# Optimization experiments

Hardware: AMD Instinct MI355X
Metric: run time of the kernel (lower is better)

Reference implementation:

```python
import jax, jax.numpy as jnp
import numpy as np

B, T_IN, T_OUT, IN_DIM, H = 65536, 30, 30, 3, 128


def _cell(xt, h, c, Wih, Whh, b):
    # PyTorch LSTM gate order: i, f, g, o
    g = xt @ Wih.T + h @ Whh.T + b  # [B, 4H]
    i, f, gg, o = jnp.split(g, 4, axis=-1)
    i = jax.nn.sigmoid(i)
    f = jax.nn.sigmoid(f)
    gg = jnp.tanh(gg)
    o = jax.nn.sigmoid(o)
    c = f * c + i * gg
    h = o * jnp.tanh(c)
    return h, c


def setup_inputs() -> dict:
    key = jax.random.key(0)
    ks = jax.random.split(key, 20)
    s = 1.0 / np.sqrt(H)
    def u(k, shape):
        return jax.random.uniform(k, shape, jnp.float32, -s, s)
    inp = {
        "x": jax.random.normal(ks[0], (B, T_IN, IN_DIM), jnp.float32),
        "enc_Wih0": u(ks[1], (4 * H, IN_DIM)),
        "enc_Whh0": u(ks[2], (4 * H, H)),
        "enc_b0": u(ks[3], (4 * H,)),
        "enc_Wih1": u(ks[4], (4 * H, H)),
        "enc_Whh1": u(ks[5], (4 * H, H)),
        "enc_b1": u(ks[6], (4 * H,)),
        "dec_Wih0": u(ks[7], (4 * H, IN_DIM)),
        "dec_Whh0": u(ks[8], (4 * H, H)),
        "dec_b0": u(ks[9], (4 * H,)),
        "dec_Wih1": u(ks[10], (4 * H, H)),
        "dec_Whh1": u(ks[11], (4 * H, H)),
        "dec_b1": u(ks[12], (4 * H,)),
        "fc_W": u(ks[13], (2 * IN_DIM, H)),
        "fc_b": u(ks[14], (2 * IN_DIM,)),
    }
    return inp


def reference(x, enc_Wih0, enc_Whh0, enc_b0, enc_Wih1, enc_Whh1, enc_b1,
              dec_Wih0, dec_Whh0, dec_b0, dec_Wih1, dec_Whh1, dec_b1,
              fc_W, fc_b):
    Bn = x.shape[0]
    z = jnp.zeros((Bn, H), x.dtype)

    # ----- encoder: 2-layer LSTM over T_in steps, keep final (h, c) -----
    def enc_step(carry, xt):
        h0, c0, h1, c1 = carry
        h0, c0 = _cell(xt, h0, c0, enc_Wih0, enc_Whh0, enc_b0)
        h1, c1 = _cell(h0, h1, c1, enc_Wih1, enc_Whh1, enc_b1)
        return (h0, c0, h1, c1), None

    xs = jnp.swapaxes(x, 0, 1)  # [T_in, B, 3]
    (h0, c0, h1, c1), _ = jax.lax.scan(enc_step, (z, z, z, z), xs)

    def dec_step(carry, _):
        h0, c0, h1, c1, inp = carry
        h0, c0 = _cell(inp, h0, c0, dec_Wih0, dec_Whh0, dec_b0)
        h1, c1 = _cell(h0, h1, c1, dec_Wih1, dec_Whh1, dec_b1)
        stats = h1 @ fc_W.T + fc_b  # [B, 6]
        mu, logvar = jnp.split(stats, 2, axis=-1)
        return (h0, c0, h1, c1, mu), (mu, logvar)

    init = (h0, c0, h1, c1, x[:, -1, :])
    _, (mus, logvars) = jax.lax.scan(dec_step, init, None, length=T_OUT)
    mu = jnp.swapaxes(mus, 0, 1)       # [B, T_out, 3]
    logvar = jnp.swapaxes(logvars, 0, 1)
    return mu, logvar
```

## Files before the change

### kernel.cpp

```cpp
#include <hip/hip_runtime.h>
#include <cstdint>

typedef short short8  __attribute__((ext_vector_type(8)));
typedef unsigned short ushort4v __attribute__((ext_vector_type(4)));
typedef float floatx4 __attribute__((ext_vector_type(4)));

#define HID    128
#define NB     32
#define TPB    512
#define NBLK   2048
#define TSTEPS 30
#define MU_OFF 5898240
#define HSZ    4096

#define L0_SZ  81920
#define L1_SZ  131072
#define ENC0_HI 0
#define ENC0_LO 81920
#define ENC1_HI 163840
#define ENC1_LO 294912
#define DEC0_HI 425984
#define DEC0_LO 507904
#define DEC1_HI 589824
#define DEC1_LO 720896

__device__ __forceinline__ float sigm(float v){
  return __builtin_amdgcn_rcpf(1.f + __expf(-v));
}
__device__ __forceinline__ float tanh_fast(float v){
  return 2.f*__builtin_amdgcn_rcpf(1.f + __expf(-2.f*v)) - 1.f;
}

__device__ __forceinline__ unsigned short f2bf(float f){
  unsigned u = __float_as_uint(f);
  u = (u + 0x7FFF + ((u>>16)&1)) >> 16;
  return (unsigned short)u;
}
__device__ __forceinline__ float bf2f(unsigned short b){
  return __uint_as_float(((unsigned)b)<<16);
}

extern "C" __global__ void __launch_bounds__(256)
prep_frag(const float* __restrict__ eWih0, const float* __restrict__ eWhh0,
          const float* __restrict__ eWih1, const float* __restrict__ eWhh1,
          const float* __restrict__ dWih0, const float* __restrict__ dWhh0,
          const float* __restrict__ dWih1, const float* __restrict__ dWhh1,
          unsigned short* __restrict__ ws)
{
  const int idx = blockIdx.x*256 + threadIdx.x;
  int i2, hi_base, lo_base, KT;
  const float* Wa; const float* Wb;
  if (idx < L0_SZ)                { i2=idx;                 hi_base=ENC0_HI; lo_base=ENC0_LO; Wa=eWhh0; Wb=eWih0; KT=5; }
  else if (idx < L0_SZ+L1_SZ)     { i2=idx-L0_SZ;           hi_base=ENC1_HI; lo_base=ENC1_LO; Wa=eWih1; Wb=eWhh1; KT=8; }
  else if (idx < 2*L0_SZ+L1_SZ)   { i2=idx-(L0_SZ+L1_SZ);   hi_base=DEC0_HI; lo_base=DEC0_LO; Wa=dWhh0; Wb=dWih0; KT=5; }
  else                            { i2=idx-(2*L0_SZ+L1_SZ); hi_base=DEC1_HI; lo_base=DEC1_LO; Wa=dWih1; Wb=dWhh1; KT=8; }
  const int jj = i2 & 7, l = (i2>>3)&63, tk = i2>>9;
  const int kt = (KT==5) ? (tk%5) : (tk&7);
  const int mt = (KT==5) ? (tk/5) : (tk>>3);
  const int row = mt*16 + (l&15);
  const int k   = kt*32 + ((l>>4)&3)*8 + jj;
  float w;
  if (KT==5) w = (k<128) ? Wa[row*128+k] : ((k<131) ? Wb[row*3 + (k-128)] : 0.f);
  else       w = (k<128) ? Wa[row*128+k] : Wb[row*128 + (k-128)];
  const unsigned short hi = f2bf(w);
  ws[hi_base + i2] = hi;
  ws[lo_base + i2] = f2bf(w - bf2f(hi));
}

extern "C" __global__ void __launch_bounds__(TPB, 4)
lstm_mfma(const float* __restrict__ x,
          const unsigned short* __restrict__ wf,
          const float* __restrict__ enc_b0, const float* __restrict__ enc_b1,
          const float* __restrict__ dec_b0, const float* __restrict__ dec_b1,
          const float* __restrict__ fc_W,  const float* __restrict__ fc_b,
          float* __restrict__ out)
{
  __shared__ unsigned short h0h[2*HSZ];
  __shared__ unsigned short h1h[2*HSZ];
  __shared__ unsigned short xbh[2*NB*8], xbl[2*NB*8];
  __shared__ unsigned short fcAh[4*512], fcAl[4*512];
  __shared__ float bias[1024];

  const int tid  = threadIdx.x;
  const int w    = tid>>6, l = tid&63;
  const int quad = (l>>4)&3, n15 = l&15;
  const int b0   = blockIdx.x*NB;

  bias[tid]       = enc_b0[tid];
  bias[512 + tid] = enc_b1[tid];
  for (int i=tid;i<2*HSZ;i+=TPB){ h0h[i]=0; h1h[i]=0; }
  xbh[tid]=0; xbl[tid]=0;
  if (w < 4){
    short8 vh, vl;
#pragma unroll
    for (int jj=0;jj<8;jj++){
      const float f = (n15<6) ? fc_W[n15*HID + w*32 + quad*8 + jj] : 0.f;
      const unsigned short hi = f2bf(f);
      vh[jj] = (short)hi;
      vl[jj] = (short)f2bf(f - bf2f(hi));
    }
    *(short8*)(fcAh + (w*64+l)*8) = vh;
    *(short8*)(fcAl + (w*64+l)*8) = vl;
  }
  float myfcb[4];
#pragma unroll
  for (int r=0;r<4;r++){
    const int oi = quad*4 + r;
    myfcb[r] = (oi<6) ? fc_b[oi] : 0.f;
  }
  __syncthreads();

  auto write_x = [&](int t, int p){
    if (tid < 96){
      const int n = tid & 31, c = tid >> 5;
      const float v = x[(size_t)(b0+n)*90 + t*3 + c];
      const unsigned short hi = f2bf(v);
      xbh[p*256 + n*8 + c] = hi;
      xbl[p*256 + n*8 + c] = f2bf(v - bf2f(hi));
    }
  };
  write_x(0, 0);
  __syncthreads();

  floatx4 acc[4][2];
  float c0[2][4], c1[2][4];
#pragma unroll
  for (int nt=0;nt<2;nt++)
#pragma unroll
    for (int r=0;r<4;r++){ c0[nt][r]=0.f; c1[nt][r]=0.f; }

  auto zacc = [&]{
    const floatx4 z = {0.f,0.f,0.f,0.f};
#pragma unroll
    for (int g=0;g<4;g++){ acc[g][0]=z; acc[g][1]=z; }
  };

  auto mv = [&](const unsigned short* __restrict__ Ahi, int KT,
                int k0, int k1, int kboff,
                const unsigned short* Bh){
#pragma unroll 1
    for (int kt=k0; kt<k1; ++kt){
      const int bo = ((((kt-kboff)*4+quad)^n15)<<3);
      short8 bh[2];
#pragma unroll
      for (int nt=0;nt<2;nt++){
        const int ro = (nt*16+n15)*128 + bo;
        bh[nt] = *(const short8*)(Bh + ro);
      }
      short8 ah[4];
#pragma unroll
      for (int g=0;g<4;g++){
        const int ao = (((g*8+w)*KT + kt)*64 + l)*8;
        ah[g] = *(const short8*)(Ahi + ao);
      }
#pragma unroll
      for (int g=0;g<4;g++){
        acc[g][0] = __builtin_amdgcn_mfma_f32_16x16x32_bf16(ah[g], bh[0], acc[g][0],0,0,0);
        acc[g][1] = __builtin_amdgcn_mfma_f32_16x16x32_bf16(ah[g], bh[1], acc[g][1],0,0,0);
      }
    }
  };

  auto mv_x = [&](const unsigned short* __restrict__ Ahi,
                  const unsigned short* Xh, const unsigned short* Xl){
    const short8 z8 = {0,0,0,0,0,0,0,0};
    short8 bh[2]={z8,z8}, bl[2]={z8,z8};
    if (quad==0){
#pragma unroll
      for (int nt=0;nt<2;nt++){
        const int ro = (nt*16+n15)*8;
        bh[nt] = *(const short8*)(Xh + ro);
        bl[nt] = *(const short8*)(Xl + ro);
      }
    }
    short8 ah[4];
#pragma unroll
    for (int g=0;g<4;g++){
      const int ao = (((g*8+w)*5 + 4)*64 + l)*8;
      ah[g] = *(const short8*)(Ahi + ao);
    }
#pragma unroll
    for (int g=0;g<4;g++){
      acc[g][0] = __builtin_amdgcn_mfma_f32_16x16x32_bf16(ah[g], bh[0], acc[g][0],0,0,0);
      acc[g][1] = __builtin_amdgcn_mfma_f32_16x16x32_bf16(ah[g], bh[1], acc[g][1],0,0,0);
    }
#pragma unroll
    for (int g=0;g<4;g++){
      acc[g][0] = __builtin_amdgcn_mfma_f32_16x16x32_bf16(ah[g], bl[0], acc[g][0],0,0,0);
      acc[g][1] = __builtin_amdgcn_mfma_f32_16x16x32_bf16(ah[g], bl[1], acc[g][1],0,0,0);
    }
  };

  auto cell = [&](float (&cst)[2][4], int boff, unsigned short* Hh){
    float hv[2][4];
#pragma unroll
    for (int nt=0;nt<2;nt++)
#pragma unroll
      for (int r=0;r<4;r++){
        const int j = w*16 + quad*4 + r;
        const float i_ = sigm(acc[0][nt][r]      + bias[boff       + j]);
        const float f_ = sigm(acc[1][nt][r]      + bias[boff + 128 + j]);
        const float g_ = tanh_fast(acc[2][nt][r] + bias[boff + 256 + j]);
        const float o_ = sigm(acc[3][nt][r]      + bias[boff + 384 + j]);
        const float c  = f_*cst[nt][r] + i_*g_;
        cst[nt][r] = c;
        hv[nt][r]  = o_*tanh_fast(c);
      }
#pragma unroll
    for (int nt=0;nt<2;nt++){
      const int jb = w*2 + (quad>>1);
      const int n  = nt*16 + n15;
      const int base = n*128 + ((jb ^ n15)<<3) + ((quad&1)<<2);
      ushort4v ph;
#pragma unroll
      for (int r=0;r<4;r++) ph[r] = f2bf(hv[nt][r]);
      *(ushort4v*)(Hh + base) = ph;
    }
  };

  auto fc = [&](int t, const unsigned short* Hh1, int xp){
    if (w < 2){
      floatx4 fa = {0.f,0.f,0.f,0.f};
#pragma unroll
      for (int kt=0;kt<4;kt++){
        const short8 ah = *(const short8*)(fcAh + (kt*64+l)*8);
        const short8 al = *(const short8*)(fcAl + (kt*64+l)*8);
        const int bo = (((kt*4+quad)^n15)<<3);
        const int ro = (w*16+n15)*128 + bo;
        const short8 bh = *(const short8*)(Hh1 + ro);
        fa = __builtin_amdgcn_mfma_f32_16x16x32_bf16(ah, bh, fa,0,0,0);
        fa = __builtin_amdgcn_mfma_f32_16x16x32_bf16(al, bh, fa,0,0,0);
      }
      const int n = w*16 + n15;
      const size_t off = (size_t)(b0+n)*90 + (size_t)t*3;
      if (quad == 0){
#pragma unroll
        for (int r=0;r<4;r++){
          const float s = fa[r] + myfcb[r];
          if (r < 3){
            out[off + r] = s;
            const unsigned short hi = f2bf(s);
            xbh[xp*256 + n*8 + r] = hi;
            xbl[xp*256 + n*8 + r] = f2bf(s - bf2f(hi));
          } else {
            out[MU_OFF + off] = s;
          }
        }
      } else if (quad == 1){
#pragma unroll
        for (int r=0;r<2;r++)
          out[MU_OFF + off + 1 + r] = fa[r] + myfcb[r];
      }
    }
  };

#pragma unroll 1
  for (int t=0; t<TSTEPS; ++t){
    const int ra = (t&1)*HSZ,  wa = HSZ - ra;
    const int xr = (t&1)*256;
    zacc();
    mv  (wf+ENC0_HI, 5, 0, 4, 0, h0h+ra);
    mv_x(wf+ENC0_HI, xbh+xr, xbl+xr);
    cell(c0, 0, h0h+wa);
    if (t+1 < TSTEPS) write_x(t+1, (t+1)&1);
    __syncthreads();
    zacc();
    mv(wf+ENC1_HI, 8, 0, 4, 0, h0h+wa);
    mv(wf+ENC1_HI, 8, 4, 8, 4, h1h+ra);
    cell(c1, 512, h1h+wa);
    __syncthreads();
  }

  bias[tid]       = dec_b0[tid];
  bias[512 + tid] = dec_b1[tid];
  __syncthreads();

#pragma unroll 1
  for (int t=0; t<TSTEPS; ++t){
    const int ra = (t&1)*HSZ,  wa = HSZ - ra;
    const int xw = (t&1)*256,  xr = 256 - xw;
    zacc();
    mv  (wf+DEC0_HI, 5, 0, 4, 0, h0h+ra);
    mv_x(wf+DEC0_HI, xbh+xr, xbl+xr);
    cell(c0, 0, h0h+wa);
    __syncthreads();
    zacc();
    mv(wf+DEC1_HI, 8, 0, 4, 0, h0h+wa);
    mv(wf+DEC1_HI, 8, 4, 8, 4, h1h+ra);
    cell(c1, 512, h1h+wa);
    __syncthreads();
    fc(t, h1h+wa, t&1);
    __syncthreads();
  }
}

extern "C" void kernel_launch(void* const* d_in, const int* in_sizes, int n_in,
                              void* d_out, int out_size, void* d_ws, size_t ws_size,
                              hipStream_t stream) {
  const float* x        = (const float*)d_in[0];
  const float* enc_Wih0 = (const float*)d_in[1];
  const float* enc_Whh0 = (const float*)d_in[2];
  const float* enc_b0   = (const float*)d_in[3];
  const float* enc_Wih1 = (const float*)d_in[4];
  const float* enc_Whh1 = (const float*)d_in[5];
  const float* enc_b1   = (const float*)d_in[6];
  const float* dec_Wih0 = (const float*)d_in[7];
  const float* dec_Whh0 = (const float*)d_in[8];
  const float* dec_b0   = (const float*)d_in[9];
  const float* dec_Wih1 = (const float*)d_in[10];
  const float* dec_Whh1 = (const float*)d_in[11];
  const float* dec_b1   = (const float*)d_in[12];
  const float* fc_W     = (const float*)d_in[13];
  const float* fc_b     = (const float*)d_in[14];
  unsigned short* ws = (unsigned short*)d_ws;
  float* out = (float*)d_out;

  prep_frag<<<1664, 256, 0, stream>>>(
      enc_Wih0, enc_Whh0, enc_Wih1, enc_Whh1,
      dec_Wih0, dec_Whh0, dec_Wih1, dec_Whh1, ws);

  lstm_mfma<<<NBLK, TPB, 0, stream>>>(
      x, ws, enc_b0, enc_b1, dec_b0, dec_b1, fc_W, fc_b, out);
}
```

Baseline: 2.657 ms.

## Reorder weight fragments per wave, cache biases in registers, pack bf16 conversion

Weight fragments are re-laid out so that each wave's four gate A-fragments for a k-tile sit contiguously, which simplifies address arithmetic in the inner loops. Gate biases are held in per-thread registers instead of being read from LDS in every cell. The h-state conversion now uses the hardware v_cvt_pk_bf16_f32 instruction, and s_setprio is raised around the MFMA bursts. These changes increase register pressure under the 4-block launch bound, and the hardware conversion's rounding may differ slightly from the manual round-to-nearest-even.

```diff
diff --git a/kernel.cpp b/kernel.cpp
--- a/kernel.cpp
+++ b/kernel.cpp
@@ -3,6 +3,7 @@
 
 typedef short short8  __attribute__((ext_vector_type(8)));
 typedef unsigned short ushort4v __attribute__((ext_vector_type(4)));
+typedef unsigned int uint2v __attribute__((ext_vector_type(2)));
 typedef float floatx4 __attribute__((ext_vector_type(4)));
 
 #define HID    128
@@ -38,6 +39,11 @@
 }
 __device__ __forceinline__ float bf2f(unsigned short b){
   return __uint_as_float(((unsigned)b)<<16);
+}
+__device__ __forceinline__ unsigned cvt_pk_bf16(float lo, float hi){
+  unsigned r;
+  asm("v_cvt_pk_bf16_f32 %0, %1, %2" : "=v"(r) : "v"(lo), "v"(hi));
+  return r;
 }
 
 extern "C" __global__ void __launch_bounds__(256)
@@ -63,8 +69,10 @@
   if (KT==5) w = (k<128) ? Wa[row*128+k] : ((k<131) ? Wb[row*3 + (k-128)] : 0.f);
   else       w = (k<128) ? Wa[row*128+k] : Wb[row*128 + (k-128)];
   const unsigned short hi = f2bf(w);
-  ws[hi_base + i2] = hi;
-  ws[lo_base + i2] = f2bf(w - bf2f(hi));
+  const int w8 = mt & 7, g = mt >> 3;
+  const int oidx = (((w8*KT + kt)*4 + g)*512) + l*8 + jj;
+  ws[hi_base + oidx] = hi;
+  ws[lo_base + oidx] = f2bf(w - bf2f(hi));
 }
 
 extern "C" __global__ void __launch_bounds__(TPB, 4)
@@ -110,6 +118,19 @@
   }
   __syncthreads();
 
+  float myb0[4][4], myb1[4][4];
+  auto load_myb = [&]{
+#pragma unroll
+    for (int g=0;g<4;g++)
+#pragma unroll
+      for (int r=0;r<4;r++){
+        const int j = g*128 + w*16 + quad*4 + r;
+        myb0[g][r] = bias[j];
+        myb1[g][r] = bias[512 + j];
+      }
+  };
+  load_myb();
+
   auto write_x = [&](int t, int p){
     if (tid < 96){
       const int n = tid & 31, c = tid >> 5;
@@ -147,17 +168,18 @@
         const int ro = (nt*16+n15)*128 + bo;
         bh[nt] = *(const short8*)(Bh + ro);
       }
+      const unsigned short* Aw = Ahi + ((w*KT + kt)*4)*512 + l*8;
       short8 ah[4];
 #pragma unroll
-      for (int g=0;g<4;g++){
-        const int ao = (((g*8+w)*KT + kt)*64 + l)*8;
-        ah[g] = *(const short8*)(Ahi + ao);
-      }
+      for (int g=0;g<4;g++)
+        ah[g] = *(const short8*)(Aw + g*512);
+      __builtin_amdgcn_s_setprio(1);
 #pragma unroll
       for (int g=0;g<4;g++){
         acc[g][0] = __builtin_amdgcn_mfma_f32_16x16x32_bf16(ah[g], bh[0], acc[g][0],0,0,0);
         acc[g][1] = __builtin_amdgcn_mfma_f32_16x16x32_bf16(ah[g], bh[1], acc[g][1],0,0,0);
       }
+      __builtin_amdgcn_s_setprio(0);
     }
   };
 
@@ -173,12 +195,12 @@
         bl[nt] = *(const short8*)(Xl + ro);
       }
     }
+    const unsigned short* Aw = Ahi + ((w*5 + 4)*4)*512 + l*8;
     short8 ah[4];
 #pragma unroll
-    for (int g=0;g<4;g++){
-      const int ao = (((g*8+w)*5 + 4)*64 + l)*8;
-      ah[g] = *(const short8*)(Ahi + ao);
-    }
+    for (int g=0;g<4;g++)
+      ah[g] = *(const short8*)(Aw + g*512);
+    __builtin_amdgcn_s_setprio(1);
 #pragma unroll
     for (int g=0;g<4;g++){
       acc[g][0] = __builtin_amdgcn_mfma_f32_16x16x32_bf16(ah[g], bh[0], acc[g][0],0,0,0);
@@ -189,19 +211,19 @@
       acc[g][0] = __builtin_amdgcn_mfma_f32_16x16x32_bf16(ah[g], bl[0], acc[g][0],0,0,0);
       acc[g][1] = __builtin_amdgcn_mfma_f32_16x16x32_bf16(ah[g], bl[1], acc[g][1],0,0,0);
     }
-  };
-
-  auto cell = [&](float (&cst)[2][4], int boff, unsigned short* Hh){
+    __builtin_amdgcn_s_setprio(0);
+  };
+
+  auto cell = [&](float (&cst)[2][4], float (&mb)[4][4], unsigned short* Hh){
     float hv[2][4];
 #pragma unroll
     for (int nt=0;nt<2;nt++)
 #pragma unroll
       for (int r=0;r<4;r++){
-        const int j = w*16 + quad*4 + r;
-        const float i_ = sigm(acc[0][nt][r]      + bias[boff       + j]);
-        const float f_ = sigm(acc[1][nt][r]      + bias[boff + 128 + j]);
-        const float g_ = tanh_fast(acc[2][nt][r] + bias[boff + 256 + j]);
-        const float o_ = sigm(acc[3][nt][r]      + bias[boff + 384 + j]);
+        const float i_ = sigm(acc[0][nt][r]      + mb[0][r]);
+        const float f_ = sigm(acc[1][nt][r]      + mb[1][r]);
+        const float g_ = tanh_fast(acc[2][nt][r] + mb[2][r]);
+        const float o_ = sigm(acc[3][nt][r]      + mb[3][r]);
         const float c  = f_*cst[nt][r] + i_*g_;
         cst[nt][r] = c;
         hv[nt][r]  = o_*tanh_fast(c);
@@ -211,10 +233,10 @@
       const int jb = w*2 + (quad>>1);
       const int n  = nt*16 + n15;
       const int base = n*128 + ((jb ^ n15)<<3) + ((quad&1)<<2);
-      ushort4v ph;
-#pragma unroll
-      for (int r=0;r<4;r++) ph[r] = f2bf(hv[nt][r]);
-      *(ushort4v*)(Hh + base) = ph;
+      uint2v pk;
+      pk[0] = cvt_pk_bf16(hv[nt][0], hv[nt][1]);
+      pk[1] = cvt_pk_bf16(hv[nt][2], hv[nt][3]);
+      *(uint2v*)(Hh + base) = pk;
     }
   };
 
@@ -261,19 +283,20 @@
     zacc();
     mv  (wf+ENC0_HI, 5, 0, 4, 0, h0h+ra);
     mv_x(wf+ENC0_HI, xbh+xr, xbl+xr);
-    cell(c0, 0, h0h+wa);
+    cell(c0, myb0, h0h+wa);
     if (t+1 < TSTEPS) write_x(t+1, (t+1)&1);
     __syncthreads();
     zacc();
     mv(wf+ENC1_HI, 8, 0, 4, 0, h0h+wa);
     mv(wf+ENC1_HI, 8, 4, 8, 4, h1h+ra);
-    cell(c1, 512, h1h+wa);
+    cell(c1, myb1, h1h+wa);
     __syncthreads();
   }
 
   bias[tid]       = dec_b0[tid];
   bias[512 + tid] = dec_b1[tid];
   __syncthreads();
+  load_myb();
 
 #pragma unroll 1
   for (int t=0; t<TSTEPS; ++t){
@@ -282,12 +305,12 @@
     zacc();
     mv  (wf+DEC0_HI, 5, 0, 4, 0, h0h+ra);
     mv_x(wf+DEC0_HI, xbh+xr, xbl+xr);
-    cell(c0, 0, h0h+wa);
+    cell(c0, myb0, h0h+wa);
     __syncthreads();
     zacc();
     mv(wf+DEC1_HI, 8, 0, 4, 0, h0h+wa);
     mv(wf+DEC1_HI, 8, 4, 8, 4, h1h+ra);
-    cell(c1, 512, h1h+wa);
+    cell(c1, myb1, h1h+wa);
     __syncthreads();
     fc(t, h1h+wa, t&1);
     __syncthreads();
```

Measured after the change: 3.024 ms. +13.8%, slower.
